# Kernel tuning notes

Measured on AMD Instinct MI355X. Metric: run time of the kernel, lower is better.

Reference implementation:

```python
import jax, jax.numpy as jnp
import numpy as np

SMOOTH = 1e-3
EPS = 1e-12


def setup_inputs() -> dict:
    key = jax.random.key(0)
    k1, k2, k3 = jax.random.split(key, 3)
    pred = jax.random.normal(k1, (1, 16, 384, 384), dtype=jnp.float32)
    labels = jax.random.randint(k2, (1, 16, 384, 384), 0, 2, dtype=jnp.int32)
    # stand-in for create_table_neighbour_code_to_surface_area((1,1,1)): 256-entry LUT
    area = jax.random.uniform(k3, (256,), dtype=jnp.float32) * 2.0
    return {"pred": pred, "labels": labels, "area": area}


def _corners(x2):
    # x2: (B, 2, Y+2, X+2) zero-padded slice pair -> (B, 8, (Y+1)*(X+1))
    # corner index k = dz*4 + dy*2 + dx, matching torch unfold(kernel=(2,2), padding=1)
    B, _, Yp, Xp = x2.shape
    Y, X = Yp - 1, Xp - 1
    cs = [x2[:, dz, dy:dy + Y, dx:dx + X]
          for dz in (0, 1) for dy in (0, 1) for dx in (0, 1)]
    return jnp.stack(cs, axis=1).reshape(B, 8, Y * X)


def _surface_dice(pred_sig, labels, area, smooth):
    B, Z, Y, X = pred_sig.shape
    # bases[i, k] = bit k of code i  (== [c=='1' for c in f'{i:08b}'[::-1]])
    bits = jnp.arange(8, dtype=jnp.int32)
    bases = ((jnp.arange(256, dtype=jnp.int32)[:, None] >> bits[None, :]) & 1).astype(jnp.float32)  # (256,8)
    n_bits = bases.sum(1)  # (256,) popcount

    # blank zero slices on both z ends + the unfold's zero padding in y/x
    Pp = jnp.pad(pred_sig, ((0, 0), (1, 1), (1, 1), (1, 1)))
    Lp = jnp.pad(labels.astype(jnp.int32), ((0, 0), (1, 1), (1, 1), (1, 1)))

    def pair(carry, i):
        num, den, vol = carry
        pz = jax.lax.dynamic_slice(Pp, (0, i, 0, 0), (B, 2, Y + 2, X + 2))
        lz = jax.lax.dynamic_slice(Lp, (0, i, 0, 0), (B, 2, Y + 2, X + 2))
        pc = _corners(pz)                      # (B, 8, Np) float
        lc = _corners(lz)                      # (B, 8, Np) int32
        byte = jnp.left_shift(lc, bits[None, :, None]).sum(axis=1)  # (B, Np) label corner code

        # basis_weights = 1 - mean_k (pc_k - bases_ik)^2, expanded so the
        # (B,256,8,Np) broadcast is never materialized
        sp2 = jnp.sum(pc * pc, axis=1)                       # (B, Np)
        cross = jnp.einsum('bkn,ik->bin', pc, bases)         # (B, 256, Np)
        bw = 1.0 - (sp2[:, None, :] + n_bits[None, :, None] - 2.0 * cross) / 8.0

        pred_byte = jnp.argmax(bw, axis=1)                   # (B, Np)
        pred_area = area[pred_byte]                          # (B, Np)
        label_area = area[byte]                              # (B, Np)
        pw = jnp.take_along_axis(bw, byte[:, None, :], axis=1)[:, 0]  # (B, Np)

        # binary_cross_entropy(unfolded_pred, unfolded_labels) per element
        lf = lc.astype(jnp.float32)
        logp = jnp.log(jnp.maximum(pc, EPS))
        log1mp = jnp.log(jnp.maximum(1.0 - pc, EPS))
        bce = -(lf * logp + (1.0 - lf) * log1mp)             # (B, 8, Np)
        interior = (byte == 0) | (byte == 255)               # (B, Np)
        v = jnp.where(interior[:, None, :], bce, 0.0).mean((1, 2))

        inter = jnp.sum(pw * label_area, axis=1)
        return (num + 2.0 * inter,
                den + label_area.sum(1) + pred_area.sum(1),
                vol + v), None

    init = (jnp.zeros((B,), jnp.float32), jnp.zeros((B,), jnp.float32), jnp.zeros((B,), jnp.float32))
    (num, den, vol), _ = jax.lax.scan(pair, init, jnp.arange(Z + 1))
    dice = 1.0 - (num + smooth) / (den + smooth)
    return dice.mean() + vol.mean()


def reference(pred, labels, area):
    return _surface_dice(jax.nn.sigmoid(pred), labels, area, SMOOTH)
```

## Files before the change

### kernel.cpp

```cpp
#include <hip/hip_runtime.h>
#include <math.h>

constexpr int ZN = 16, YN = 384, XN = 384;
constexpr int NZ = 17, NY = 385, NX = 385;
constexpr int NP = NY * NX;
constexpr int NROWS = NZ * NY;
constexpr int BLOCKS = (NROWS + 3) / 4;

typedef float F2 __attribute__((ext_vector_type(2)));
typedef int   I2 __attribute__((ext_vector_type(2)));

__global__ __launch_bounds__(256) void sd_main(
        const float* __restrict__ pred,
        const int*   __restrict__ labels,
        const float* __restrict__ area,
        float*       __restrict__ partial)
{
    __shared__ float s_area[256];
    {
        const int t = threadIdx.x;
        const int own = t >> 4, prv = t & 15;
        int code = 0;
#pragma unroll
        for (int r = 0; r < 4; ++r)
            code |= (((prv >> r) & 1) << (2 * r)) | (((own >> r) & 1) << (2 * r + 1));
        s_area[t] = area[code];
    }
    __syncthreads();

    const int lane = threadIdx.x & 63;
    const int wid  = blockIdx.x * 4 + (threadIdx.x >> 6);

    float num = 0.f, den = 0.f, vol = 0.f;

    if (wid < NROWS) {
        const int z = wid / NY;
        const int y = wid - z * NY;

        float s[6][4];
        float q[6]  = {0.f, 0.f, 0.f, 0.f, 0.f, 0.f};
        int   cb[6] = {0, 0, 0, 0, 0, 0};
        const int xb = 6 * lane;

#pragma unroll
        for (int r = 0; r < 4; ++r) {
            const int zz = z - 1 + (r >> 1);
            const int yy = y - 1 + (r & 1);
            const bool rv = ((unsigned)zz < (unsigned)ZN) & ((unsigned)yy < (unsigned)YN);
            if (rv) {
                const int base = (zz * YN + yy) * XN + xb;
                const F2* pp = (const F2*)(pred + base);
                const I2* lp = (const I2*)(labels + base);
                const F2 pa_ = pp[0], pb_ = pp[1], pc_ = pp[2];
                const I2 la_ = lp[0], lb_ = lp[1], lc_ = lp[2];
                const float p[6] = {pa_.x, pa_.y, pb_.x, pb_.y, pc_.x, pc_.y};
                const int   l[6] = {la_.x, la_.y, lb_.x, lb_.y, lc_.x, lc_.y};
#pragma unroll
                for (int j = 0; j < 6; ++j) {
                    const float sv = __fdividef(1.f, 1.f + __expf(-p[j]));
                    s[j][r] = sv;
                    const float d = sv - (float)l[j];
                    q[j] = fmaf(d, d, q[j]);
                    cb[j] |= (l[j] << r) | ((int)(p[j] > 0.f) << (r + 4));
                }
            } else {
#pragma unroll
                for (int j = 0; j < 6; ++j) s[j][r] = 0.f;
            }
        }

        auto node = [&](const float* sp, float qp, int bp,
                        const float* so, float qo, int bo) {
            const int idxL = ((bo & 15) << 4) | (bp & 15);
            const int idxP = (bo & 0xF0) | (bp >> 4);
            const float la = s_area[idxL];
            const float pa = s_area[idxP];
            const float pw = 1.f - (qp + qo) * 0.125f;
            num = fmaf(2.f * la, pw, num);
            den += la + pa;
            if (idxL == 0 || idxL == 255) {
                const bool one = (idxL == 255);
                float b = 0.f;
#pragma unroll
                for (int r = 0; r < 4; ++r) {
                    const float up = one ? sp[r] : 1.f - sp[r];
                    const float uo = one ? so[r] : 1.f - so[r];
                    b += __logf(fmaxf(up, 1e-12f)) + __logf(fmaxf(uo, 1e-12f));
                }
                vol -= b;
            }
        };

        float ps[4]; float pq; int pb;
#pragma unroll
        for (int r = 0; r < 4; ++r) ps[r] = __shfl_up(s[5][r], 1);
        pq = __shfl_up(q[5], 1);
        pb = __shfl_up(cb[5], 1);
        if (lane == 0) { ps[0] = ps[1] = ps[2] = ps[3] = 0.f; pq = 0.f; pb = 0; }

        node(ps,   pq,   pb,    s[0], q[0], cb[0]);
        node(s[0], q[0], cb[0], s[1], q[1], cb[1]);
        node(s[1], q[1], cb[1], s[2], q[2], cb[2]);
        node(s[2], q[2], cb[2], s[3], q[3], cb[3]);
        node(s[3], q[3], cb[3], s[4], q[4], cb[4]);
        node(s[4], q[4], cb[4], s[5], q[5], cb[5]);
        if (lane == 63) {
            const float zs[4] = {0.f, 0.f, 0.f, 0.f};
            node(s[5], q[5], cb[5], zs, 0.f, 0);
        }
    }

#pragma unroll
    for (int off = 32; off > 0; off >>= 1) {
        num += __shfl_down(num, off);
        den += __shfl_down(den, off);
        vol += __shfl_down(vol, off);
    }
    __shared__ float sn[4], sd_[4], sv[4];
    const int w = threadIdx.x >> 6;
    if (lane == 0) { sn[w] = num; sd_[w] = den; sv[w] = vol; }
    __syncthreads();
    if (threadIdx.x == 0) {
        partial[blockIdx.x]              = sn[0] + sn[1] + sn[2] + sn[3];
        partial[BLOCKS + blockIdx.x]     = sd_[0] + sd_[1] + sd_[2] + sd_[3];
        partial[2 * BLOCKS + blockIdx.x] = sv[0] + sv[1] + sv[2] + sv[3];
    }
}

__global__ __launch_bounds__(256) void sd_final(
        const float* __restrict__ partial, float* __restrict__ out)
{
    double n = 0.0, d = 0.0, v = 0.0;
    for (int b = threadIdx.x; b < BLOCKS; b += 256) {
        n += (double)partial[b];
        d += (double)partial[BLOCKS + b];
        v += (double)partial[2 * BLOCKS + b];
    }
#pragma unroll
    for (int off = 32; off > 0; off >>= 1) {
        n += __shfl_down(n, off);
        d += __shfl_down(d, off);
        v += __shfl_down(v, off);
    }
    __shared__ double sn[4], sd_[4], sv[4];
    const int lane = threadIdx.x & 63, w = threadIdx.x >> 6;
    if (lane == 0) { sn[w] = n; sd_[w] = d; sv[w] = v; }
    __syncthreads();
    if (threadIdx.x == 0) {
        const double num = sn[0] + sn[1] + sn[2] + sn[3];
        const double den = sd_[0] + sd_[1] + sd_[2] + sd_[3];
        const double vol = (sv[0] + sv[1] + sv[2] + sv[3]) / (8.0 * (double)NP);
        const double dice = 1.0 - (num + 1e-3) / (den + 1e-3);
        out[0] = (float)(dice + vol);
    }
}

extern "C" void kernel_launch(void* const* d_in, const int* in_sizes, int n_in,
                              void* d_out, int out_size, void* d_ws, size_t ws_size,
                              hipStream_t stream)
{
    const float* pred   = (const float*)d_in[0];
    const int*   labels = (const int*)d_in[1];
    const float* area   = (const float*)d_in[2];
    float* out     = (float*)d_out;
    float* partial = (float*)d_ws;

    sd_main<<<BLOCKS, 256, 0, stream>>>(pred, labels, area, partial);
    sd_final<<<1, 256, 0, stream>>>(partial, out);
}
```

Before: 86.70 us.

## Map one output row per block with one thread per column via LDS exchange

```diff
diff --git a/kernel.cpp b/kernel.cpp
--- a/kernel.cpp
+++ b/kernel.cpp
@@ -5,20 +5,24 @@
 constexpr int NZ = 17, NY = 385, NX = 385;
 constexpr int NP = NY * NX;
 constexpr int NROWS = NZ * NY;
-constexpr int BLOCKS = (NROWS + 3) / 4;
+constexpr int TPB = 384;
 
-typedef float F2 __attribute__((ext_vector_type(2)));
-typedef int   I2 __attribute__((ext_vector_type(2)));
+__device__ __forceinline__ float sigm(float p) {
+    return __fdividef(1.f, 1.f + __expf(-p));
+}
 
-__global__ __launch_bounds__(256) void sd_main(
+__global__ __launch_bounds__(TPB) void sd_main(
         const float* __restrict__ pred,
         const int*   __restrict__ labels,
         const float* __restrict__ area,
         float*       __restrict__ partial)
 {
     __shared__ float s_area[256];
-    {
-        const int t = threadIdx.x;
+    __shared__ float s_col[385 * 6];
+    __shared__ float rn[6], rd[6], rv[6];
+
+    const int t = threadIdx.x;
+    if (t < 256) {
         const int own = t >> 4, prv = t & 15;
         int code = 0;
 #pragma unroll
@@ -26,87 +30,78 @@
             code |= (((prv >> r) & 1) << (2 * r)) | (((own >> r) & 1) << (2 * r + 1));
         s_area[t] = area[code];
     }
+
+    const int row = blockIdx.x;
+    const int z = row / NY;
+    const int y = row - z * NY;
+
+    float s[4] = {0.f, 0.f, 0.f, 0.f};
+    float q = 0.f;
+    int bits = 0;
+    {
+        const bool vz0 = (z >= 1), vz1 = (z <= ZN - 1);
+        const bool vy0 = (y >= 1), vy1 = (y <= YN - 1);
+        const bool val[4] = { vz0 && vy0, vz0 && vy1, vz1 && vy0, vz1 && vy1 };
+        const int  off[4] = {
+            ((z - 1) * YN + (y - 1)) * XN + t,
+            ((z - 1) * YN + y)       * XN + t,
+            (z * YN + (y - 1))       * XN + t,
+            (z * YN + y)             * XN + t };
+#pragma unroll
+        for (int r = 0; r < 4; ++r) {
+            if (val[r]) {
+                const float p = pred[off[r]];
+                const int   l = labels[off[r]];
+                const float sv = sigm(p);
+                s[r] = sv;
+                const float d = sv - (float)l;
+                q = fmaf(d, d, q);
+                bits |= (l << r) | ((int)(p > 0.f) << (r + 4));
+            }
+        }
+    }
+    {
+        float* e = &s_col[(t + 1) * 6];
+        if (t == 383) e = &s_col[0];
+        if (t == 383) {
+            e[0] = 0.f; e[1] = 0.f; e[2] = 0.f; e[3] = 0.f; e[4] = 0.f;
+            ((int*)e)[5] = 0;
+        } else {
+            e[0] = s[0]; e[1] = s[1]; e[2] = s[2]; e[3] = s[3]; e[4] = q;
+            ((int*)e)[5] = bits;
+        }
+    }
     __syncthreads();
 
-    const int lane = threadIdx.x & 63;
-    const int wid  = blockIdx.x * 4 + (threadIdx.x >> 6);
-
     float num = 0.f, den = 0.f, vol = 0.f;
-
-    if (wid < NROWS) {
-        const int z = wid / NY;
-        const int y = wid - z * NY;
-
-        float s[6][4];
-        float q[6]  = {0.f, 0.f, 0.f, 0.f, 0.f, 0.f};
-        int   cb[6] = {0, 0, 0, 0, 0, 0};
-        const int xb = 6 * lane;
-
+    auto node = [&](const float* sp, float qp, int bp,
+                    const float* so, float qo, int bo) {
+        const int idxL = ((bo & 15) << 4) | (bp & 15);
+        const int idxP = ((bo >> 4) << 4) | (bp >> 4);
+        const float la = s_area[idxL];
+        const float pa = s_area[idxP];
+        num = fmaf(2.f * la, 1.f - (qp + qo) * 0.125f, num);
+        den += la + pa;
+        if (idxL == 0 || idxL == 255) {
+            const bool one = (idxL == 255);
+            float b = 0.f;
 #pragma unroll
-        for (int r = 0; r < 4; ++r) {
-            const int zz = z - 1 + (r >> 1);
-            const int yy = y - 1 + (r & 1);
-            const bool rv = ((unsigned)zz < (unsigned)ZN) & ((unsigned)yy < (unsigned)YN);
-            if (rv) {
-                const int base = (zz * YN + yy) * XN + xb;
-                const F2* pp = (const F2*)(pred + base);
-                const I2* lp = (const I2*)(labels + base);
-                const F2 pa_ = pp[0], pb_ = pp[1], pc_ = pp[2];
-                const I2 la_ = lp[0], lb_ = lp[1], lc_ = lp[2];
-                const float p[6] = {pa_.x, pa_.y, pb_.x, pb_.y, pc_.x, pc_.y};
-                const int   l[6] = {la_.x, la_.y, lb_.x, lb_.y, lc_.x, lc_.y};
-#pragma unroll
-                for (int j = 0; j < 6; ++j) {
-                    const float sv = __fdividef(1.f, 1.f + __expf(-p[j]));
-                    s[j][r] = sv;
-                    const float d = sv - (float)l[j];
-                    q[j] = fmaf(d, d, q[j]);
-                    cb[j] |= (l[j] << r) | ((int)(p[j] > 0.f) << (r + 4));
-                }
-            } else {
-#pragma unroll
-                for (int j = 0; j < 6; ++j) s[j][r] = 0.f;
+            for (int r = 0; r < 4; ++r) {
+                b += __logf(fmaxf(one ? sp[r] : 1.f - sp[r], 1e-12f))
+                   + __logf(fmaxf(one ? so[r] : 1.f - so[r], 1e-12f));
             }
+            vol -= b;
         }
-
-        auto node = [&](const float* sp, float qp, int bp,
-                        const float* so, float qo, int bo) {
-            const int idxL = ((bo & 15) << 4) | (bp & 15);
-            const int idxP = (bo & 0xF0) | (bp >> 4);
-            const float la = s_area[idxL];
-            const float pa = s_area[idxP];
-            const float pw = 1.f - (qp + qo) * 0.125f;
-            num = fmaf(2.f * la, pw, num);
-            den += la + pa;
-            if (idxL == 0 || idxL == 255) {
-                const bool one = (idxL == 255);
-                float b = 0.f;
-#pragma unroll
-                for (int r = 0; r < 4; ++r) {
-                    const float up = one ? sp[r] : 1.f - sp[r];
-                    const float uo = one ? so[r] : 1.f - so[r];
-                    b += __logf(fmaxf(up, 1e-12f)) + __logf(fmaxf(uo, 1e-12f));
-                }
-                vol -= b;
-            }
-        };
-
-        float ps[4]; float pq; int pb;
-#pragma unroll
-        for (int r = 0; r < 4; ++r) ps[r] = __shfl_up(s[5][r], 1);
-        pq = __shfl_up(q[5], 1);
-        pb = __shfl_up(cb[5], 1);
-        if (lane == 0) { ps[0] = ps[1] = ps[2] = ps[3] = 0.f; pq = 0.f; pb = 0; }
-
-        node(ps,   pq,   pb,    s[0], q[0], cb[0]);
-        node(s[0], q[0], cb[0], s[1], q[1], cb[1]);
-        node(s[1], q[1], cb[1], s[2], q[2], cb[2]);
-        node(s[2], q[2], cb[2], s[3], q[3], cb[3]);
-        node(s[3], q[3], cb[3], s[4], q[4], cb[4]);
-        node(s[4], q[4], cb[4], s[5], q[5], cb[5]);
-        if (lane == 63) {
+    };
+    {
+        const float* e = &s_col[t * 6];
+        float ps[4] = { e[0], e[1], e[2], e[3] };
+        const float pq = e[4];
+        const int   pb = ((const int*)e)[5];
+        node(ps, pq, pb, s, q, bits);
+        if (t == 383) {
             const float zs[4] = {0.f, 0.f, 0.f, 0.f};
-            node(s[5], q[5], cb[5], zs, 0.f, 0);
+            node(s, q, bits, zs, 0.f, 0);
         }
     }
 
@@ -116,14 +111,16 @@
         den += __shfl_down(den, off);
         vol += __shfl_down(vol, off);
     }
-    __shared__ float sn[4], sd_[4], sv[4];
-    const int w = threadIdx.x >> 6;
-    if (lane == 0) { sn[w] = num; sd_[w] = den; sv[w] = vol; }
+    const int lane = t & 63, w = t >> 6;
+    if (lane == 0) { rn[w] = num; rd[w] = den; rv[w] = vol; }
     __syncthreads();
-    if (threadIdx.x == 0) {
-        partial[blockIdx.x]              = sn[0] + sn[1] + sn[2] + sn[3];
-        partial[BLOCKS + blockIdx.x]     = sd_[0] + sd_[1] + sd_[2] + sd_[3];
-        partial[2 * BLOCKS + blockIdx.x] = sv[0] + sv[1] + sv[2] + sv[3];
+    if (t == 0) {
+        float n = 0.f, d = 0.f, v = 0.f;
+#pragma unroll
+        for (int i = 0; i < 6; ++i) { n += rn[i]; d += rd[i]; v += rv[i]; }
+        partial[row]             = n;
+        partial[NROWS + row]     = d;
+        partial[2 * NROWS + row] = v;
     }
 }
 
@@ -131,10 +128,10 @@
         const float* __restrict__ partial, float* __restrict__ out)
 {
     double n = 0.0, d = 0.0, v = 0.0;
-    for (int b = threadIdx.x; b < BLOCKS; b += 256) {
+    for (int b = threadIdx.x; b < NROWS; b += 256) {
         n += (double)partial[b];
-        d += (double)partial[BLOCKS + b];
-        v += (double)partial[2 * BLOCKS + b];
+        d += (double)partial[NROWS + b];
+        v += (double)partial[2 * NROWS + b];
     }
 #pragma unroll
     for (int off = 32; off > 0; off >>= 1) {
@@ -165,6 +162,6 @@
     float* out     = (float*)d_out;
     float* partial = (float*)d_ws;
 
-    sd_main<<<BLOCKS, 256, 0, stream>>>(pred, labels, area, partial);
+    sd_main<<<NROWS, TPB, 0, stream>>>(pred, labels, area, partial);
     sd_final<<<1, 256, 0, stream>>>(partial, out);
 }
```

Result: slower. 96.89 us (+11.8%).

## Split each row across two waves with three columns per lane and 512-thread blocks

Applied to the files above, without the earlier changes.

```diff
diff --git a/kernel.cpp b/kernel.cpp
--- a/kernel.cpp
+++ b/kernel.cpp
@@ -5,20 +5,24 @@
 constexpr int NZ = 17, NY = 385, NX = 385;
 constexpr int NP = NY * NX;
 constexpr int NROWS = NZ * NY;
-constexpr int BLOCKS = (NROWS + 3) / 4;
+constexpr int NWAVES = NROWS * 2;
+constexpr int TPB = 512;
+constexpr int BLOCKS = (NWAVES + 7) / 8;
 
-typedef float F2 __attribute__((ext_vector_type(2)));
-typedef int   I2 __attribute__((ext_vector_type(2)));
+__device__ __forceinline__ float sigm(float p) {
+    return __fdividef(1.f, 1.f + __expf(-p));
+}
 
-__global__ __launch_bounds__(256) void sd_main(
+__global__ __launch_bounds__(TPB, 8) void sd_main(
         const float* __restrict__ pred,
         const int*   __restrict__ labels,
         const float* __restrict__ area,
         float*       __restrict__ partial)
 {
     __shared__ float s_area[256];
-    {
-        const int t = threadIdx.x;
+    __shared__ float rn[8], rd[8], rv[8];
+    const int t = threadIdx.x;
+    if (t < 256) {
         const int own = t >> 4, prv = t & 15;
         int code = 0;
 #pragma unroll
@@ -28,36 +32,58 @@
     }
     __syncthreads();
 
-    const int lane = threadIdx.x & 63;
-    const int wid  = blockIdx.x * 4 + (threadIdx.x >> 6);
+    const int lane = t & 63;
+    const int wid  = blockIdx.x * 8 + (t >> 6);
 
     float num = 0.f, den = 0.f, vol = 0.f;
 
-    if (wid < NROWS) {
-        const int z = wid / NY;
-        const int y = wid - z * NY;
+    if (wid < NWAVES) {
+        const int row = wid >> 1;
+        const int c   = wid & 1;
+        const int z = row / NY;
+        const int y = row - z * NY;
 
-        float s[6][4];
-        float q[6]  = {0.f, 0.f, 0.f, 0.f, 0.f, 0.f};
-        int   cb[6] = {0, 0, 0, 0, 0, 0};
-        const int xb = 6 * lane;
-
+        bool rval[4]; int base[4];
 #pragma unroll
         for (int r = 0; r < 4; ++r) {
             const int zz = z - 1 + (r >> 1);
             const int yy = y - 1 + (r & 1);
-            const bool rv = ((unsigned)zz < (unsigned)ZN) & ((unsigned)yy < (unsigned)YN);
-            if (rv) {
-                const int base = (zz * YN + yy) * XN + xb;
-                const F2* pp = (const F2*)(pred + base);
-                const I2* lp = (const I2*)(labels + base);
-                const F2 pa_ = pp[0], pb_ = pp[1], pc_ = pp[2];
-                const I2 la_ = lp[0], lb_ = lp[1], lc_ = lp[2];
-                const float p[6] = {pa_.x, pa_.y, pb_.x, pb_.y, pc_.x, pc_.y};
-                const int   l[6] = {la_.x, la_.y, lb_.x, lb_.y, lc_.x, lc_.y};
+            rval[r] = ((unsigned)zz < (unsigned)ZN) & ((unsigned)yy < (unsigned)YN);
+            base[r] = (zz * YN + yy) * XN;
+        }
+
+        float gs[4] = {0.f, 0.f, 0.f, 0.f};
+        float gq = 0.f; int gb = 0;
+        if (c == 1 && lane == 0) {
 #pragma unroll
-                for (int j = 0; j < 6; ++j) {
-                    const float sv = __fdividef(1.f, 1.f + __expf(-p[j]));
+            for (int r = 0; r < 4; ++r) {
+                if (rval[r]) {
+                    const float p = pred[base[r] + 191];
+                    const int   l = labels[base[r] + 191];
+                    const float sv = sigm(p);
+                    gs[r] = sv;
+                    const float d = sv - (float)l;
+                    gq = fmaf(d, d, gq);
+                    gb |= (l << r) | ((int)(p > 0.f) << (r + 4));
+                }
+            }
+        }
+
+        const int xb = c * 192 + 3 * lane;
+        float s[3][4];
+        float q[3]  = {0.f, 0.f, 0.f};
+        int   cb[3] = {0, 0, 0};
+#pragma unroll
+        for (int r = 0; r < 4; ++r) {
+            if (rval[r]) {
+                const float* pp = pred + base[r] + xb;
+                const int*   lp = labels + base[r] + xb;
+                float p[3]; int l[3];
+#pragma unroll
+                for (int j = 0; j < 3; ++j) { p[j] = pp[j]; l[j] = lp[j]; }
+#pragma unroll
+                for (int j = 0; j < 3; ++j) {
+                    const float sv = sigm(p[j]);
                     s[j][r] = sv;
                     const float d = sv - (float)l[j];
                     q[j] = fmaf(d, d, q[j]);
@@ -65,7 +91,7 @@
                 }
             } else {
 #pragma unroll
-                for (int j = 0; j < 6; ++j) s[j][r] = 0.f;
+                for (int j = 0; j < 3; ++j) s[j][r] = 0.f;
             }
         }
 
@@ -75,17 +101,15 @@
             const int idxP = (bo & 0xF0) | (bp >> 4);
             const float la = s_area[idxL];
             const float pa = s_area[idxP];
-            const float pw = 1.f - (qp + qo) * 0.125f;
-            num = fmaf(2.f * la, pw, num);
+            num = fmaf(2.f * la, 1.f - (qp + qo) * 0.125f, num);
             den += la + pa;
             if (idxL == 0 || idxL == 255) {
                 const bool one = (idxL == 255);
                 float b = 0.f;
 #pragma unroll
                 for (int r = 0; r < 4; ++r) {
-                    const float up = one ? sp[r] : 1.f - sp[r];
-                    const float uo = one ? so[r] : 1.f - so[r];
-                    b += __logf(fmaxf(up, 1e-12f)) + __logf(fmaxf(uo, 1e-12f));
+                    b += __logf(fmaxf(one ? sp[r] : 1.f - sp[r], 1e-12f))
+                       + __logf(fmaxf(one ? so[r] : 1.f - so[r], 1e-12f));
                 }
                 vol -= b;
             }
@@ -93,20 +117,21 @@
 
         float ps[4]; float pq; int pb;
 #pragma unroll
-        for (int r = 0; r < 4; ++r) ps[r] = __shfl_up(s[5][r], 1);
-        pq = __shfl_up(q[5], 1);
-        pb = __shfl_up(cb[5], 1);
-        if (lane == 0) { ps[0] = ps[1] = ps[2] = ps[3] = 0.f; pq = 0.f; pb = 0; }
+        for (int r = 0; r < 4; ++r) ps[r] = __shfl_up(s[2][r], 1);
+        pq = __shfl_up(q[2], 1);
+        pb = __shfl_up(cb[2], 1);
+        if (lane == 0) {
+#pragma unroll
+            for (int r = 0; r < 4; ++r) ps[r] = gs[r];
+            pq = gq; pb = gb;
+        }
 
         node(ps,   pq,   pb,    s[0], q[0], cb[0]);
         node(s[0], q[0], cb[0], s[1], q[1], cb[1]);
         node(s[1], q[1], cb[1], s[2], q[2], cb[2]);
-        node(s[2], q[2], cb[2], s[3], q[3], cb[3]);
-        node(s[3], q[3], cb[3], s[4], q[4], cb[4]);
-        node(s[4], q[4], cb[4], s[5], q[5], cb[5]);
-        if (lane == 63) {
+        if (c == 1 && lane == 63) {
             const float zs[4] = {0.f, 0.f, 0.f, 0.f};
-            node(s[5], q[5], cb[5], zs, 0.f, 0);
+            node(s[2], q[2], cb[2], zs, 0.f, 0);
         }
     }
 
@@ -116,14 +141,16 @@
         den += __shfl_down(den, off);
         vol += __shfl_down(vol, off);
     }
-    __shared__ float sn[4], sd_[4], sv[4];
-    const int w = threadIdx.x >> 6;
-    if (lane == 0) { sn[w] = num; sd_[w] = den; sv[w] = vol; }
+    const int w = t >> 6;
+    if (lane == 0) { rn[w] = num; rd[w] = den; rv[w] = vol; }
     __syncthreads();
-    if (threadIdx.x == 0) {
-        partial[blockIdx.x]              = sn[0] + sn[1] + sn[2] + sn[3];
-        partial[BLOCKS + blockIdx.x]     = sd_[0] + sd_[1] + sd_[2] + sd_[3];
-        partial[2 * BLOCKS + blockIdx.x] = sv[0] + sv[1] + sv[2] + sv[3];
+    if (t == 0) {
+        float n = 0.f, d = 0.f, v = 0.f;
+#pragma unroll
+        for (int i = 0; i < 8; ++i) { n += rn[i]; d += rd[i]; v += rv[i]; }
+        partial[blockIdx.x]              = n;
+        partial[BLOCKS + blockIdx.x]     = d;
+        partial[2 * BLOCKS + blockIdx.x] = v;
     }
 }
 
@@ -165,6 +192,6 @@
     float* out     = (float*)d_out;
     float* partial = (float*)d_ws;
 
-    sd_main<<<BLOCKS, 256, 0, stream>>>(pred, labels, area, partial);
+    sd_main<<<BLOCKS, TPB, 0, stream>>>(pred, labels, area, partial);
     sd_final<<<1, 256, 0, stream>>>(partial, out);
 }
```

After: 86.57 us. Within noise of the previous version (-0.2%).

## Use strided per-lane column mapping with rotating shuffle chain instead of contiguous chunks

Applied to the files above, without the earlier changes.

```diff
diff --git a/kernel.cpp b/kernel.cpp
--- a/kernel.cpp
+++ b/kernel.cpp
@@ -7,8 +7,9 @@
 constexpr int NROWS = NZ * NY;
 constexpr int BLOCKS = (NROWS + 3) / 4;
 
-typedef float F2 __attribute__((ext_vector_type(2)));
-typedef int   I2 __attribute__((ext_vector_type(2)));
+__device__ __forceinline__ float sigm(float p) {
+    return __fdividef(1.f, 1.f + __expf(-p));
+}
 
 __global__ __launch_bounds__(256) void sd_main(
         const float* __restrict__ pred,
@@ -29,7 +30,7 @@
     __syncthreads();
 
     const int lane = threadIdx.x & 63;
-    const int wid  = blockIdx.x * 4 + (threadIdx.x >> 6);
+    const int wid = __builtin_amdgcn_readfirstlane(blockIdx.x * 4 + (threadIdx.x >> 6));
 
     float num = 0.f, den = 0.f, vol = 0.f;
 
@@ -37,36 +38,13 @@
         const int z = wid / NY;
         const int y = wid - z * NY;
 
-        float s[6][4];
-        float q[6]  = {0.f, 0.f, 0.f, 0.f, 0.f, 0.f};
-        int   cb[6] = {0, 0, 0, 0, 0, 0};
-        const int xb = 6 * lane;
-
+        bool rval[4]; int base[4];
 #pragma unroll
         for (int r = 0; r < 4; ++r) {
             const int zz = z - 1 + (r >> 1);
             const int yy = y - 1 + (r & 1);
-            const bool rv = ((unsigned)zz < (unsigned)ZN) & ((unsigned)yy < (unsigned)YN);
-            if (rv) {
-                const int base = (zz * YN + yy) * XN + xb;
-                const F2* pp = (const F2*)(pred + base);
-                const I2* lp = (const I2*)(labels + base);
-                const F2 pa_ = pp[0], pb_ = pp[1], pc_ = pp[2];
-                const I2 la_ = lp[0], lb_ = lp[1], lc_ = lp[2];
-                const float p[6] = {pa_.x, pa_.y, pb_.x, pb_.y, pc_.x, pc_.y};
-                const int   l[6] = {la_.x, la_.y, lb_.x, lb_.y, lc_.x, lc_.y};
-#pragma unroll
-                for (int j = 0; j < 6; ++j) {
-                    const float sv = __fdividef(1.f, 1.f + __expf(-p[j]));
-                    s[j][r] = sv;
-                    const float d = sv - (float)l[j];
-                    q[j] = fmaf(d, d, q[j]);
-                    cb[j] |= (l[j] << r) | ((int)(p[j] > 0.f) << (r + 4));
-                }
-            } else {
-#pragma unroll
-                for (int j = 0; j < 6; ++j) s[j][r] = 0.f;
-            }
+            rval[r] = ((unsigned)zz < (unsigned)ZN) & ((unsigned)yy < (unsigned)YN);
+            base[r] = (zz * YN + yy) * XN;
         }
 
         auto node = [&](const float* sp, float qp, int bp,
@@ -75,38 +53,71 @@
             const int idxP = (bo & 0xF0) | (bp >> 4);
             const float la = s_area[idxL];
             const float pa = s_area[idxP];
-            const float pw = 1.f - (qp + qo) * 0.125f;
-            num = fmaf(2.f * la, pw, num);
+            num = fmaf(2.f * la, 1.f - (qp + qo) * 0.125f, num);
             den += la + pa;
             if (idxL == 0 || idxL == 255) {
                 const bool one = (idxL == 255);
                 float b = 0.f;
 #pragma unroll
                 for (int r = 0; r < 4; ++r) {
-                    const float up = one ? sp[r] : 1.f - sp[r];
-                    const float uo = one ? so[r] : 1.f - so[r];
-                    b += __logf(fmaxf(up, 1e-12f)) + __logf(fmaxf(uo, 1e-12f));
+                    b += __logf(fmaxf(one ? sp[r] : 1.f - sp[r], 1e-12f))
+                       + __logf(fmaxf(one ? so[r] : 1.f - so[r], 1e-12f));
                 }
                 vol -= b;
             }
         };
 
-        float ps[4]; float pq; int pb;
+        const int src = (lane + 63) & 63;
+        const bool l0 = (lane == 0);
+
+        float rp_s[4] = {0.f, 0.f, 0.f, 0.f};
+        float rp_q = 0.f; int rp_b = 0;
+        float last_s[4]; float last_q = 0.f; int last_b = 0;
+
 #pragma unroll
-        for (int r = 0; r < 4; ++r) ps[r] = __shfl_up(s[5][r], 1);
-        pq = __shfl_up(q[5], 1);
-        pb = __shfl_up(cb[5], 1);
-        if (lane == 0) { ps[0] = ps[1] = ps[2] = ps[3] = 0.f; pq = 0.f; pb = 0; }
-
-        node(ps,   pq,   pb,    s[0], q[0], cb[0]);
-        node(s[0], q[0], cb[0], s[1], q[1], cb[1]);
-        node(s[1], q[1], cb[1], s[2], q[2], cb[2]);
-        node(s[2], q[2], cb[2], s[3], q[3], cb[3]);
-        node(s[3], q[3], cb[3], s[4], q[4], cb[4]);
-        node(s[4], q[4], cb[4], s[5], q[5], cb[5]);
+        for (int j = 0; j < 6; ++j) {
+            const int xo = j * 64 + lane;
+            float s[4] = {0.f, 0.f, 0.f, 0.f};
+            float q = 0.f; int b = 0;
+#pragma unroll
+            for (int r = 0; r < 4; ++r) {
+                if (rval[r]) {
+                    const float p = pred[base[r] + xo];
+                    const int   l = labels[base[r] + xo];
+                    const float sv = sigm(p);
+                    s[r] = sv;
+                    const float d = sv - (float)l;
+                    q = fmaf(d, d, q);
+                    b |= (l << r) | ((int)(p > 0.f) << (r + 4));
+                }
+            }
+            float ps[4], pq; int pb;
+#pragma unroll
+            for (int r = 0; r < 4; ++r) {
+                const float ro = __shfl(s[r], src);
+                ps[r] = l0 ? rp_s[r] : ro;
+                rp_s[r] = ro;
+            }
+            {
+                const float ro = __shfl(q, src);
+                pq = l0 ? rp_q : ro;
+                rp_q = ro;
+            }
+            {
+                const int ro = __shfl(b, src);
+                pb = l0 ? rp_b : ro;
+                rp_b = ro;
+            }
+            node(ps, pq, pb, s, q, b);
+            if (j == 5) {
+#pragma unroll
+                for (int r = 0; r < 4; ++r) last_s[r] = s[r];
+                last_q = q; last_b = b;
+            }
+        }
         if (lane == 63) {
             const float zs[4] = {0.f, 0.f, 0.f, 0.f};
-            node(s[5], q[5], cb[5], zs, 0.f, 0);
+            node(last_s, last_q, last_b, zs, 0.f, 0);
         }
     }
 
@@ -116,14 +127,14 @@
         den += __shfl_down(den, off);
         vol += __shfl_down(vol, off);
     }
-    __shared__ float sn[4], sd_[4], sv[4];
+    __shared__ float rn[4], rd[4], rv[4];
     const int w = threadIdx.x >> 6;
-    if (lane == 0) { sn[w] = num; sd_[w] = den; sv[w] = vol; }
+    if (lane == 0) { rn[w] = num; rd[w] = den; rv[w] = vol; }
     __syncthreads();
     if (threadIdx.x == 0) {
-        partial[blockIdx.x]              = sn[0] + sn[1] + sn[2] + sn[3];
-        partial[BLOCKS + blockIdx.x]     = sd_[0] + sd_[1] + sd_[2] + sd_[3];
-        partial[2 * BLOCKS + blockIdx.x] = sv[0] + sv[1] + sv[2] + sv[3];
+        partial[blockIdx.x]              = rn[0] + rn[1] + rn[2] + rn[3];
+        partial[BLOCKS + blockIdx.x]     = rd[0] + rd[1] + rd[2] + rd[3];
+        partial[2 * BLOCKS + blockIdx.x] = rv[0] + rv[1] + rv[2] + rv[3];
     }
 }
 
```

Measured after the change: 85.74 us, median of 2. No clear change (-1.1%).
